# Optimization experiments

Measured on AMD Instinct MI355X. Metric: run time of the kernel, lower is better.

Reference implementation:

```python
import jax, jax.numpy as jnp
import numpy as np
from math import sqrt

N, L, IN, OUT, H = 100000, 5, 256, 256, 4
DH = OUT // H
RED = OUT // 16  # SE reduction
SCALE = 1.0 / sqrt(OUT)  # note: module scales by 1/sqrt(out_size), not per-head dim


def setup_inputs() -> dict:
    key = jax.random.key(0)
    ks = jax.random.split(key, 12)
    std = 0.02
    return {
        "x": jax.random.normal(ks[0], (N, L, IN), dtype=jnp.float32),
        "Wq": jax.random.normal(ks[1], (H, IN, DH), dtype=jnp.float32) * std,
        "bq": jax.random.normal(ks[2], (H, DH), dtype=jnp.float32) * std,
        "Wk": jax.random.normal(ks[3], (H, IN, DH), dtype=jnp.float32) * std,
        "bk": jax.random.normal(ks[4], (H, DH), dtype=jnp.float32) * std,
        "Wv": jax.random.normal(ks[5], (H, IN, DH), dtype=jnp.float32) * std,
        "bv": jax.random.normal(ks[6], (H, DH), dtype=jnp.float32) * std,
        "W1": jax.random.normal(ks[7], (OUT, RED), dtype=jnp.float32) * std,
        "b1": jax.random.normal(ks[8], (RED,), dtype=jnp.float32) * std,
        "W2": jax.random.normal(ks[9], (RED, OUT), dtype=jnp.float32) * std,
        "b2": jax.random.normal(ks[10], (OUT,), dtype=jnp.float32) * std,
    }


def reference(x, Wq, bq, Wk, bk, Wv, bv, W1, b1, W2, b2):
    # Batched per-head QKV projections: [H, N, L, DH]
    Q = jnp.einsum("nli,hid->hnld", x, Wq) + bq[:, None, None, :]
    K = jnp.einsum("nli,hid->hnld", x, Wk) + bk[:, None, None, :]
    V = jnp.einsum("nli,hid->hnld", x, Wv) + bv[:, None, None, :]
    # attention over the small layer dim L
    attn = jnp.einsum("hnld,hnmd->hnlm", Q, K) * SCALE
    alpha = jax.nn.softmax(attn, axis=-1)  # softmax over dim=2 of [N,L,L] == last axis here
    z = jnp.einsum("hnlm,hnmd->hnld", alpha, V)
    # concat heads -> [N, L, OUT]
    z = jnp.transpose(z, (1, 2, 0, 3)).reshape(N, L, OUT)
    # SE block: squeeze over layer dim, excite with 2-layer MLP gate
    s = z.mean(axis=1, keepdims=True)                      # [N,1,OUT]
    g = jax.nn.sigmoid(jax.nn.relu(s @ W1 + b1) @ W2 + b2)  # [N,1,OUT]
    z = g * z
    return z.mean(axis=1)  # [N, OUT]
```

## Files before the change

### kernel.cpp

```cpp
#include <hip/hip_runtime.h>

typedef unsigned int uint;
typedef unsigned short ushort;

typedef short bfrag __attribute__((ext_vector_type(8)));
typedef float f32x4 __attribute__((ext_vector_type(4)));

__device__ __forceinline__ ushort f2bf(float f) {
  uint u = __float_as_uint(f);
  u = (u + 0x7FFFu + ((u >> 16) & 1u)) >> 16;
  return (ushort)u;
}
__device__ __forceinline__ float bf2f(ushort h) {
  return __uint_as_float(((uint)h) << 16);
}
__device__ __forceinline__ float sigmoidf(float t) {
  return 1.0f / (1.0f + __expf(-t));
}

__global__ void prep_kernel(const float* __restrict__ Wq, const float* __restrict__ Wk,
                            const float* __restrict__ Wv, const float* __restrict__ W1,
                            ushort* __restrict__ wb, float* __restrict__ w1t) {
  int idx = blockIdx.x * 256 + threadIdx.x;
  if (idx < 196608) {
    int j    = idx & 7;
    int lane = (idx >> 3) & 63;
    int kk   = (idx >> 9) & 7;
    int gnt  = idx >> 12;
    int head = gnt / 12;
    int nh   = (gnt % 12) * 16 + (lane & 15);
    int k    = kk * 32 + (lane >> 4) * 8 + j;
    int sel  = nh >> 6, d = nh & 63;
    const float* W = (sel == 0) ? Wq : ((sel == 1) ? Wk : Wv);
    wb[idx] = f2bf(W[(head * 256 + k) * 64 + d]);
  }
  if (idx < 4096) {
    int j = idx >> 8, c = idx & 255;
    w1t[idx] = W1[c * 16 + j];
  }
}

__global__ __launch_bounds__(256, 2)
void fused_kernel(const float* __restrict__ x,
                  const float* __restrict__ bq, const float* __restrict__ bk,
                  const float* __restrict__ bv,
                  const ushort* __restrict__ wb, const float* __restrict__ w1t,
                  const float* __restrict__ b1, const float* __restrict__ W2,
                  const float* __restrict__ b2, float* __restrict__ out) {
  __shared__ ushort xlds[20480];
  __shared__ ushort qkv[15360];
  __shared__ ushort sbuf[4096];
  __shared__ float  scratch[496];

  const int tid  = threadIdx.x;
  const int lane = tid & 63;
  const int wave = tid >> 6;
  const int ln   = lane & 15;
  const int quad = lane >> 4;
  const int blk  = blockIdx.x;

  {
    const float* xb = x + (size_t)blk * 20480;
#pragma unroll
    for (int it = 0; it < 20; ++it) {
      int f = it * 1024 + tid * 4;
      float4 v = *(const float4*)(xb + f);
      int row = f >> 8;
      int col = f & 255;
      int ch = col >> 3;
      int half = (col >> 2) & 1;
      int phys = ch ^ (row & 7);
      uint2 p;
      p.x = (uint)f2bf(v.x) | ((uint)f2bf(v.y) << 16);
      p.y = (uint)f2bf(v.z) | ((uint)f2bf(v.w) << 16);
      *(uint2*)(&xlds[row * 256 + phys * 8 + half * 4]) = p;
    }
  }
  __syncthreads();

  const int sample = tid >> 4;
  const int u      = tid & 15;
  float* sc  = scratch;
  float* wgt = scratch + 416;

  for (int head = 0; head < 4; ++head) {
    f32x4 acc[5][3];
#pragma unroll
    for (int mt = 0; mt < 5; ++mt)
#pragma unroll
      for (int nt = 0; nt < 3; ++nt)
        acc[mt][nt] = (f32x4){0.f, 0.f, 0.f, 0.f};

#pragma unroll
    for (int kk = 0; kk < 8; ++kk) {
      bfrag a[5], b[3];
      int cb = kk * 4 + quad;
#pragma unroll
      for (int mt = 0; mt < 5; ++mt) {
        int row = mt * 16 + ln;
        int off = row * 256 + ((cb ^ (row & 7)) << 3);
        a[mt] = *(const bfrag*)(&xlds[off]);
      }
#pragma unroll
      for (int nt = 0; nt < 3; ++nt) {
        int goff = (((head * 12 + wave * 3 + nt) * 8 + kk) * 64 + lane) * 8;
        b[nt] = *(const bfrag*)(wb + goff);
      }
#pragma unroll
      for (int nt = 0; nt < 3; ++nt)
#pragma unroll
        for (int mt = 0; mt < 5; ++mt)
          acc[mt][nt] = __builtin_amdgcn_mfma_f32_16x16x32_bf16(a[mt], b[nt], acc[mt][nt], 0, 0, 0);
    }

#pragma unroll
    for (int nt = 0; nt < 3; ++nt) {
      int ncol = wave * 48 + nt * 16 + ln;
      int sel = ncol >> 6, d = ncol & 63;
      const float* bp = (sel == 0) ? bq : ((sel == 1) ? bk : bv);
      float bias = bp[head * 64 + d];
#pragma unroll
      for (int mt = 0; mt < 5; ++mt) {
#pragma unroll
        for (int r = 0; r < 4; ++r) {
          int row = mt * 16 + quad * 4 + r;
          int e = row * 192 + (((ncol >> 3) ^ (row & 7)) << 3) + (ncol & 7);
          qkv[e] = f2bf(acc[mt][nt][r] + bias);
        }
      }
    }
    __syncthreads();

    if (u < 5) {
      int rq = sample * 5 + u;
      float S[5] = {0.f, 0.f, 0.f, 0.f, 0.f};
      for (int d = 0; d < 64; d += 4) {
        float q0, q1, q2, q3;
        {
          uint2 v = *(const uint2*)(&qkv[rq * 192 + (((d >> 3) ^ (rq & 7)) << 3) + (d & 7)]);
          q0 = bf2f((ushort)(v.x & 0xffff)); q1 = bf2f((ushort)(v.x >> 16));
          q2 = bf2f((ushort)(v.y & 0xffff)); q3 = bf2f((ushort)(v.y >> 16));
        }
#pragma unroll
        for (int m = 0; m < 5; ++m) {
          int rk = sample * 5 + m;
          int col = 64 + d;
          uint2 v = *(const uint2*)(&qkv[rk * 192 + (((col >> 3) ^ (rk & 7)) << 3) + (col & 7)]);
          S[m] += q0 * bf2f((ushort)(v.x & 0xffff)) + q1 * bf2f((ushort)(v.x >> 16))
                + q2 * bf2f((ushort)(v.y & 0xffff)) + q3 * bf2f((ushort)(v.y >> 16));
        }
      }
      float mx = S[0] * 0.0625f;
#pragma unroll
      for (int m = 1; m < 5; ++m) mx = fmaxf(mx, S[m] * 0.0625f);
      float e[5], sum = 0.f;
#pragma unroll
      for (int m = 0; m < 5; ++m) { e[m] = __expf(S[m] * 0.0625f - mx); sum += e[m]; }
      float inv = 1.0f / sum;
#pragma unroll
      for (int m = 0; m < 5; ++m) sc[sample * 26 + u * 5 + m] = e[m] * inv;
    }
    __syncthreads();

    if (u < 5) {
      float wsum = 0.f;
#pragma unroll
      for (int l = 0; l < 5; ++l) wsum += sc[sample * 26 + l * 5 + u];
      wgt[sample * 5 + u] = wsum * 0.2f;
    }
    __syncthreads();

    {
      int dbase = u * 4;
      float a0 = 0.f, a1 = 0.f, a2 = 0.f, a3 = 0.f;
#pragma unroll
      for (int m = 0; m < 5; ++m) {
        int row = sample * 5 + m;
        float wv = wgt[sample * 5 + m];
        int col = 128 + dbase;
        uint2 v = *(const uint2*)(&qkv[row * 192 + (((col >> 3) ^ (row & 7)) << 3) + (col & 7)]);
        a0 += wv * bf2f((ushort)(v.x & 0xffff));
        a1 += wv * bf2f((ushort)(v.x >> 16));
        a2 += wv * bf2f((ushort)(v.y & 0xffff));
        a3 += wv * bf2f((ushort)(v.y >> 16));
      }
      uint2 p;
      p.x = (uint)f2bf(a0) | ((uint)f2bf(a1) << 16);
      p.y = (uint)f2bf(a2) | ((uint)f2bf(a3) << 16);
      *(uint2*)(&sbuf[sample * 256 + head * 64 + dbase]) = p;
    }
    __syncthreads();
  }

  {
    float acc = b1[u];
    const float* wr = w1t + u * 256;
#pragma unroll 4
    for (int c = 0; c < 256; c += 4) {
      uint2 sv = *(const uint2*)(&sbuf[sample * 256 + c]);
      float4 wv = *(const float4*)(wr + c);
      acc += bf2f((ushort)(sv.x & 0xffff)) * wv.x + bf2f((ushort)(sv.x >> 16)) * wv.y
           + bf2f((ushort)(sv.y & 0xffff)) * wv.z + bf2f((ushort)(sv.y >> 16)) * wv.w;
    }
    float* rbuf = scratch;
    rbuf[sample * 16 + u] = fmaxf(acc, 0.f);
  }
  __syncthreads();

  {
    const float* rbuf = scratch;
    float g[16];
#pragma unroll
    for (int i = 0; i < 16; ++i) g[i] = b2[u * 16 + i];
#pragma unroll
    for (int j = 0; j < 16; ++j) {
      float rj = rbuf[sample * 16 + j];
      const float* w2r = W2 + j * 256 + u * 16;
#pragma unroll
      for (int i = 0; i < 16; i += 4) {
        float4 wv = *(const float4*)(w2r + i);
        g[i + 0] += rj * wv.x; g[i + 1] += rj * wv.y;
        g[i + 2] += rj * wv.z; g[i + 3] += rj * wv.w;
      }
    }
    float* ob = out + ((size_t)blk * 16 + sample) * 256 + u * 16;
#pragma unroll
    for (int i = 0; i < 16; i += 4) {
      int c = u * 16 + i;
      uint2 sv = *(const uint2*)(&sbuf[sample * 256 + c]);
      float4 ov;
      ov.x = sigmoidf(g[i + 0]) * bf2f((ushort)(sv.x & 0xffff));
      ov.y = sigmoidf(g[i + 1]) * bf2f((ushort)(sv.x >> 16));
      ov.z = sigmoidf(g[i + 2]) * bf2f((ushort)(sv.y & 0xffff));
      ov.w = sigmoidf(g[i + 3]) * bf2f((ushort)(sv.y >> 16));
      *(float4*)(ob + i) = ov;
    }
  }
}

extern "C" void kernel_launch(void* const* d_in, const int* in_sizes, int n_in,
                              void* d_out, int out_size, void* d_ws, size_t ws_size,
                              hipStream_t stream) {
  const float* x  = (const float*)d_in[0];
  const float* Wq = (const float*)d_in[1];
  const float* bq = (const float*)d_in[2];
  const float* Wk = (const float*)d_in[3];
  const float* bk = (const float*)d_in[4];
  const float* Wv = (const float*)d_in[5];
  const float* bv = (const float*)d_in[6];
  const float* W1 = (const float*)d_in[7];
  const float* b1 = (const float*)d_in[8];
  const float* W2 = (const float*)d_in[9];
  const float* b2 = (const float*)d_in[10];

  ushort* wb  = (ushort*)d_ws;
  float*  w1t = (float*)((char*)d_ws + 393216);

  prep_kernel<<<768, 256, 0, stream>>>(Wq, Wk, Wv, W1, wb, w1t);
  fused_kernel<<<6250, 256, 0, stream>>>(x, bq, bk, bv, wb, w1t, b1, W2, b2,
                                         (float*)d_out);
}
```

Measured before the change: 1.258 ms.

## Compute attention scores with MFMA and reduce softmax via wave shuffles

```diff
diff --git a/kernel.cpp b/kernel.cpp
--- a/kernel.cpp
+++ b/kernel.cpp
@@ -14,8 +14,13 @@
 __device__ __forceinline__ float bf2f(ushort h) {
   return __uint_as_float(((uint)h) << 16);
 }
+__device__ __forceinline__ uint cvt_pk_bf16(float lo, float hi) {
+  uint r;
+  asm("v_cvt_pk_bf16_f32 %0, %1, %2" : "=v"(r) : "v"(lo), "v"(hi));
+  return r;
+}
 __device__ __forceinline__ float sigmoidf(float t) {
-  return 1.0f / (1.0f + __expf(-t));
+  return __builtin_amdgcn_rcpf(1.0f + __expf(-t));
 }
 
 __global__ void prep_kernel(const float* __restrict__ Wq, const float* __restrict__ Wk,
@@ -48,9 +53,9 @@
                   const float* __restrict__ b1, const float* __restrict__ W2,
                   const float* __restrict__ b2, float* __restrict__ out) {
   __shared__ ushort xlds[20480];
-  __shared__ ushort qkv[15360];
+  __shared__ ushort qkv[16000];
   __shared__ ushort sbuf[4096];
-  __shared__ float  scratch[496];
+  __shared__ float  wgt[128];
 
   const int tid  = threadIdx.x;
   const int lane = tid & 63;
@@ -71,8 +76,8 @@
       int half = (col >> 2) & 1;
       int phys = ch ^ (row & 7);
       uint2 p;
-      p.x = (uint)f2bf(v.x) | ((uint)f2bf(v.y) << 16);
-      p.y = (uint)f2bf(v.z) | ((uint)f2bf(v.w) << 16);
+      p.x = cvt_pk_bf16(v.x, v.y);
+      p.y = cvt_pk_bf16(v.z, v.w);
       *(uint2*)(&xlds[row * 256 + phys * 8 + half * 4]) = p;
     }
   }
@@ -80,8 +85,16 @@
 
   const int sample = tid >> 4;
   const int u      = tid & 15;
-  float* sc  = scratch;
-  float* wgt = scratch + 416;
+
+  const int sl   = ln >> 3;
+  const int mm   = ln & 7;
+  const int qsel = quad - (sl << 1);
+  const bool lo  = (qsel == 0), hi = (qsel == 1);
+  const bool lv  = (mm < 5);
+  int r0 = (wave * 4 + sl) * 5 + mm;      if (r0 > 79) r0 = 79;
+  int r1 = (wave * 4 + 2 + sl) * 5 + mm;  if (r1 > 79) r1 = 79;
+  const int bQ0 = r0 * 400 + quad * 16;
+  const int bQ1 = r1 * 400 + quad * 16;
 
   for (int head = 0; head < 4; ++head) {
     f32x4 acc[5][3];
@@ -110,111 +123,117 @@
       for (int nt = 0; nt < 3; ++nt)
 #pragma unroll
         for (int mt = 0; mt < 5; ++mt)
-          acc[mt][nt] = __builtin_amdgcn_mfma_f32_16x16x32_bf16(a[mt], b[nt], acc[mt][nt], 0, 0, 0);
+          acc[mt][nt] = __builtin_amdgcn_mfma_f32_16x16x32_bf16(b[nt], a[mt], acc[mt][nt], 0, 0, 0);
     }
 
 #pragma unroll
     for (int nt = 0; nt < 3; ++nt) {
-      int ncol = wave * 48 + nt * 16 + ln;
-      int sel = ncol >> 6, d = ncol & 63;
+      int nq = wave * 48 + nt * 16 + quad * 4;
+      int sel = nq >> 6, d0 = nq & 63;
       const float* bp = (sel == 0) ? bq : ((sel == 1) ? bk : bv);
-      float bias = bp[head * 64 + d];
+      float4 bias = *(const float4*)(bp + head * 64 + d0);
 #pragma unroll
       for (int mt = 0; mt < 5; ++mt) {
-#pragma unroll
-        for (int r = 0; r < 4; ++r) {
-          int row = mt * 16 + quad * 4 + r;
-          int e = row * 192 + (((ncol >> 3) ^ (row & 7)) << 3) + (ncol & 7);
-          qkv[e] = f2bf(acc[mt][nt][r] + bias);
+        int xr = mt * 16 + ln;
+        uint2 p;
+        p.x = cvt_pk_bf16(acc[mt][nt][0] + bias.x, acc[mt][nt][1] + bias.y);
+        p.y = cvt_pk_bf16(acc[mt][nt][2] + bias.z, acc[mt][nt][3] + bias.w);
+        *(uint2*)(&qkv[xr * 200 + nq]) = p;
+      }
+    }
+    __syncthreads();
+
+    f32x4 s0 = {0.f, 0.f, 0.f, 0.f}, s1 = {0.f, 0.f, 0.f, 0.f};
+    {
+      const char* qb = (const char*)qkv;
+#pragma unroll
+      for (int kk = 0; kk < 2; ++kk) {
+        bfrag qf0 = *(const bfrag*)(qb + bQ0 + kk * 64);
+        bfrag kf0 = *(const bfrag*)(qb + bQ0 + 128 + kk * 64);
+        bfrag qf1 = *(const bfrag*)(qb + bQ1 + kk * 64);
+        bfrag kf1 = *(const bfrag*)(qb + bQ1 + 128 + kk * 64);
+        s0 = __builtin_amdgcn_mfma_f32_16x16x32_bf16(kf0, qf0, s0, 0, 0, 0);
+        s1 = __builtin_amdgcn_mfma_f32_16x16x32_bf16(kf1, qf1, s1, 0, 0, 0);
+      }
+    }
+
+    auto attn_tile = [&](const f32x4 sS, const int t) {
+      float t0 = sS[0] * 0.0625f, t1 = sS[1] * 0.0625f;
+      float t2 = sS[2] * 0.0625f, t3 = sS[3] * 0.0625f;
+      float pm = lo ? fmaxf(fmaxf(t0, t1), fmaxf(t2, t3)) : (hi ? t0 : -1e30f);
+      pm = fmaxf(pm, __shfl_xor(pm, 16));
+      pm = fmaxf(pm, __shfl_xor(pm, 32));
+      float e0 = __expf(t0 - pm), e1 = __expf(t1 - pm);
+      float e2 = __expf(t2 - pm), e3 = __expf(t3 - pm);
+      float ps = lo ? (e0 + e1 + e2 + e3) : (hi ? e0 : 0.f);
+      ps += __shfl_xor(ps, 16);
+      ps += __shfl_xor(ps, 32);
+      float inv = 0.2f * __builtin_amdgcn_rcpf(ps);
+      float c0 = ((lo || hi) && lv) ? e0 * inv : 0.f;
+      float c1 = (lo && lv) ? e1 * inv : 0.f;
+      float c2 = (lo && lv) ? e2 * inv : 0.f;
+      float c3 = (lo && lv) ? e3 * inv : 0.f;
+      c0 += __shfl_xor(c0, 1); c0 += __shfl_xor(c0, 2); c0 += __shfl_xor(c0, 4);
+      c1 += __shfl_xor(c1, 1); c1 += __shfl_xor(c1, 2); c1 += __shfl_xor(c1, 4);
+      c2 += __shfl_xor(c2, 1); c2 += __shfl_xor(c2, 2); c2 += __shfl_xor(c2, 4);
+      c3 += __shfl_xor(c3, 1); c3 += __shfl_xor(c3, 2); c3 += __shfl_xor(c3, 4);
+      int smp = wave * 4 + t * 2 + sl;
+      if (mm == 0) {
+        if (qsel == 0) {
+          *(float4*)(wgt + smp * 8) = make_float4(c0, c1, c2, c3);
+        } else if (qsel == 1) {
+          wgt[smp * 8 + 4] = c0;
         }
       }
-    }
-    __syncthreads();
-
-    if (u < 5) {
-      int rq = sample * 5 + u;
-      float S[5] = {0.f, 0.f, 0.f, 0.f, 0.f};
-      for (int d = 0; d < 64; d += 4) {
-        float q0, q1, q2, q3;
-        {
-          uint2 v = *(const uint2*)(&qkv[rq * 192 + (((d >> 3) ^ (rq & 7)) << 3) + (d & 7)]);
-          q0 = bf2f((ushort)(v.x & 0xffff)); q1 = bf2f((ushort)(v.x >> 16));
-          q2 = bf2f((ushort)(v.y & 0xffff)); q3 = bf2f((ushort)(v.y >> 16));
-        }
-#pragma unroll
-        for (int m = 0; m < 5; ++m) {
-          int rk = sample * 5 + m;
-          int col = 64 + d;
-          uint2 v = *(const uint2*)(&qkv[rk * 192 + (((col >> 3) ^ (rk & 7)) << 3) + (col & 7)]);
-          S[m] += q0 * bf2f((ushort)(v.x & 0xffff)) + q1 * bf2f((ushort)(v.x >> 16))
-                + q2 * bf2f((ushort)(v.y & 0xffff)) + q3 * bf2f((ushort)(v.y >> 16));
-        }
-      }
-      float mx = S[0] * 0.0625f;
-#pragma unroll
-      for (int m = 1; m < 5; ++m) mx = fmaxf(mx, S[m] * 0.0625f);
-      float e[5], sum = 0.f;
-#pragma unroll
-      for (int m = 0; m < 5; ++m) { e[m] = __expf(S[m] * 0.0625f - mx); sum += e[m]; }
-      float inv = 1.0f / sum;
-#pragma unroll
-      for (int m = 0; m < 5; ++m) sc[sample * 26 + u * 5 + m] = e[m] * inv;
-    }
-    __syncthreads();
-
-    if (u < 5) {
-      float wsum = 0.f;
-#pragma unroll
-      for (int l = 0; l < 5; ++l) wsum += sc[sample * 26 + l * 5 + u];
-      wgt[sample * 5 + u] = wsum * 0.2f;
-    }
-    __syncthreads();
+    };
+    attn_tile(s0, 0);
+    attn_tile(s1, 1);
+    __builtin_amdgcn_wave_barrier();
 
     {
-      int dbase = u * 4;
+      float4 w03 = *(const float4*)(wgt + sample * 8);
+      float w4 = wgt[sample * 8 + 4];
       float a0 = 0.f, a1 = 0.f, a2 = 0.f, a3 = 0.f;
 #pragma unroll
       for (int m = 0; m < 5; ++m) {
-        int row = sample * 5 + m;
-        float wv = wgt[sample * 5 + m];
-        int col = 128 + dbase;
-        uint2 v = *(const uint2*)(&qkv[row * 192 + (((col >> 3) ^ (row & 7)) << 3) + (col & 7)]);
+        float wv = (m == 0) ? w03.x : (m == 1) ? w03.y : (m == 2) ? w03.z
+                 : (m == 3) ? w03.w : w4;
+        uint2 v = *(const uint2*)(&qkv[(sample * 5 + m) * 200 + 128 + u * 4]);
         a0 += wv * bf2f((ushort)(v.x & 0xffff));
         a1 += wv * bf2f((ushort)(v.x >> 16));
         a2 += wv * bf2f((ushort)(v.y & 0xffff));
         a3 += wv * bf2f((ushort)(v.y >> 16));
       }
       uint2 p;
-      p.x = (uint)f2bf(a0) | ((uint)f2bf(a1) << 16);
-      p.y = (uint)f2bf(a2) | ((uint)f2bf(a3) << 16);
-      *(uint2*)(&sbuf[sample * 256 + head * 64 + dbase]) = p;
+      p.x = cvt_pk_bf16(a0, a1);
+      p.y = cvt_pk_bf16(a2, a3);
+      *(uint2*)(&sbuf[sample * 256 + head * 64 + u * 4]) = p;
     }
     __syncthreads();
   }
 
+  float rse;
   {
-    float acc = b1[u];
+    float accv = b1[u];
     const float* wr = w1t + u * 256;
 #pragma unroll 4
     for (int c = 0; c < 256; c += 4) {
       uint2 sv = *(const uint2*)(&sbuf[sample * 256 + c]);
       float4 wv = *(const float4*)(wr + c);
-      acc += bf2f((ushort)(sv.x & 0xffff)) * wv.x + bf2f((ushort)(sv.x >> 16)) * wv.y
-           + bf2f((ushort)(sv.y & 0xffff)) * wv.z + bf2f((ushort)(sv.y >> 16)) * wv.w;
-    }
-    float* rbuf = scratch;
-    rbuf[sample * 16 + u] = fmaxf(acc, 0.f);
-  }
-  __syncthreads();
+      accv += bf2f((ushort)(sv.x & 0xffff)) * wv.x + bf2f((ushort)(sv.x >> 16)) * wv.y
+            + bf2f((ushort)(sv.y & 0xffff)) * wv.z + bf2f((ushort)(sv.y >> 16)) * wv.w;
+    }
+    rse = fmaxf(accv, 0.f);
+  }
 
   {
-    const float* rbuf = scratch;
     float g[16];
 #pragma unroll
     for (int i = 0; i < 16; ++i) g[i] = b2[u * 16 + i];
+    const int lbase = tid & 48;
 #pragma unroll
     for (int j = 0; j < 16; ++j) {
-      float rj = rbuf[sample * 16 + j];
+      float rj = __shfl(rse, lbase | j, 64);
       const float* w2r = W2 + j * 256 + u * 16;
 #pragma unroll
       for (int i = 0; i < 16; i += 4) {
```

New measurement: 1.169 ms. -7.0%, faster.
